# Kernel tuning notes

Measured on AMD Instinct MI355X. Metric: run time of the kernel, lower is better.

Reference implementation:

```python
import jax, jax.numpy as jnp
import numpy as np

B, T, D, H = 2, 2048, 2048, 16
HD = D // H  # 128
HALF = HD // 2  # 64


def _apply_rotary(x, cos, sin):
    """x: (B,H,T,HD); cos/sin: (T, HD//2). Interleaved rotation matching torch ref."""
    half = x.shape[-1] // 2
    x1, x2 = x[..., :half], x[..., half:]
    c = cos[None, None, :, :]
    s = sin[None, None, :, :]
    # stack on last axis then flatten -> out[...,2i]=x1*c-x2*s, out[...,2i+1]=x1*s+x2*c
    return jnp.stack([x1 * c - x2 * s, x1 * s + x2 * c], axis=-1).reshape(x.shape)


def setup_inputs() -> dict:
    key = jax.random.key(0)
    k1, k2, k3 = jax.random.split(key, 3)
    x = jax.random.normal(k1, (B, T, D), dtype=jnp.float32)
    # realistic RoPE tables: theta = 10000^{-2i/HD}
    inv_freq = 1.0 / (10000.0 ** (np.arange(0, HALF, dtype=np.float32) * 2.0 / HD))
    ang = np.arange(T, dtype=np.float32)[:, None] * inv_freq[None, :]  # (T, HALF)
    cos = jnp.asarray(np.cos(ang), dtype=jnp.float32)
    sin = jnp.asarray(np.sin(ang), dtype=jnp.float32)
    Wqkv = jax.random.normal(k2, (D, 3 * D), dtype=jnp.float32) * (D ** -0.5)
    Wproj = jax.random.normal(k3, (D, D), dtype=jnp.float32) * (D ** -0.5)
    return {"x": x, "cos": cos, "sin": sin, "Wqkv": Wqkv, "Wproj": Wproj}


def reference(x, cos, sin, Wqkv, Wproj):
    b, t, d = x.shape
    qkv = (x @ Wqkv).reshape(b, t, 3, H, HD)
    q = jnp.transpose(qkv[:, :, 0], (0, 2, 1, 3))  # (B,H,T,HD)
    k = jnp.transpose(qkv[:, :, 1], (0, 2, 1, 3))
    v = jnp.transpose(qkv[:, :, 2], (0, 2, 1, 3))
    q = _apply_rotary(q, cos, sin)
    k = _apply_rotary(k, cos, sin)
    scale = 1.0 / jnp.sqrt(jnp.asarray(HD, dtype=x.dtype))
    scores = jnp.einsum("bhqd,bhkd->bhqk", q, k) * scale
    causal = jnp.tril(jnp.ones((t, t), dtype=bool))
    scores = jnp.where(causal[None, None], scores, jnp.finfo(x.dtype).min)
    attn = jax.nn.softmax(scores, axis=-1)
    out = jnp.einsum("bhqk,bhkd->bhqd", attn, v)
    out = jnp.transpose(out, (0, 2, 1, 3)).reshape(b, t, d)
    return out @ Wproj
```

## Files before the change

### kernel.cpp

```cpp
#include <hip/hip_runtime.h>
#include <hip/hip_bf16.h>

#define B_  2
#define T_  2048
#define D_  2048
#define H_  16
#define HD_ 128
#define NT_ 4096
#define D3_ 6144

typedef __bf16 bf16;
typedef _Float16 f16;
typedef bf16 bf16x2 __attribute__((ext_vector_type(2)));
typedef bf16 bf16x4 __attribute__((ext_vector_type(4)));
typedef bf16 bf16x8 __attribute__((ext_vector_type(8)));
typedef f16  f16x2  __attribute__((ext_vector_type(2)));
typedef f16  f16x4  __attribute__((ext_vector_type(4)));
typedef float floatx4 __attribute__((ext_vector_type(4)));

__device__ __forceinline__ void gl_lds16(const void* g, void* l) {
    __builtin_amdgcn_global_load_lds((const __attribute__((address_space(1))) void*)g,
                                     (__attribute__((address_space(3))) void*)l, 16, 0, 0);
}

__global__ __launch_bounds__(256) void k_prep(const float* __restrict__ x,
                                              const float* __restrict__ Wqkv, const float* __restrict__ Wproj,
                                              bf16* __restrict__ xb, bf16* __restrict__ WqkvT, bf16* __restrict__ WprojT) {
    int blk = blockIdx.x;
    int tid = threadIdx.x;
    if (blk < 8192) {
        int i = blk * 256 + tid;
        float4 v = ((const float4*)x)[i];
        bf16x4 o = { (bf16)v.x, (bf16)v.y, (bf16)v.z, (bf16)v.w };
        ((bf16x4*)xb)[i] = o;
        return;
    }
    __shared__ float tile[64][65];
    const float* in; bf16* out; int C, bx;
    if (blk < 8192 + 3072) { bx = blk - 8192; in = Wqkv; out = WqkvT; C = D3_; }
    else                   { bx = blk - 8192 - 3072; in = Wproj; out = WprojT; C = D_; }
    const int R = D_;
    int nbx = C / 64;
    int c0 = (bx % nbx) * 64, r0 = (bx / nbx) * 64;
#pragma unroll
    for (int i = 0; i < 16; i++) {
        int idx = tid + i * 256, r = idx >> 6, c = idx & 63;
        tile[r][c] = in[(size_t)(r0 + r) * C + (c0 + c)];
    }
    __syncthreads();
#pragma unroll
    for (int i = 0; i < 16; i++) {
        int idx = tid + i * 256, r = idx >> 6, c = idx & 63;
        out[(size_t)(c0 + r) * R + (r0 + c)] = (bf16)tile[c][r];
    }
}

__global__ __launch_bounds__(512, 1) void k_gemm_qkv(const bf16* __restrict__ A, const bf16* __restrict__ Bt,
                                                     const float* __restrict__ cosp, const float* __restrict__ sinp,
                                                     bf16* __restrict__ Qg, bf16* __restrict__ Kg, f16* __restrict__ VTg) {
    __shared__ bf16 smem[3 * 24576];
    const int tid = threadIdx.x, wid = tid >> 6, lane = tid & 63;
    const int quad = lane >> 4, l16 = lane & 15;
    const int n0 = blockIdx.x * 128, m0 = blockIdx.y * 256;
    const int wr = (wid >> 1) * 64, wc = (wid & 1) * 64;
    const bf16* Ablk = A + (size_t)m0 * D_;
    const bf16* Bblk = Bt + (size_t)n0 * D_;
    const int sgch = (lane & 7) ^ (lane >> 3);
    const int aHalf = (wid >> 2) * 8192;
    const int rAbase = ((wid >> 1) & 1) * 64;
    const int coA = (rAbase + l16) * 64;
    const int coB = 16384 + (wc + l16) * 64;
    floatx4 acc[4][4] = {};

#define QKV_STAGE(KT, BUFO, JJ) do {                                                    \
        int cI_ = (JJ) * 512 + wid * 64 + lane;                                         \
        const bf16* gsrc_;                                                              \
        if ((JJ) < 4) gsrc_ = Ablk + (size_t)(cI_ >> 3) * D_ + (KT) * 64 + sgch * 8;    \
        else          gsrc_ = Bblk + (size_t)((cI_ >> 3) - 256) * D_ + (KT) * 64 + sgch * 8; \
        gl_lds16(gsrc_, smem + (BUFO) + ((JJ) * 512 + wid * 64) * 8);                   \
    } while (0)

#pragma unroll
    for (int j = 0; j < 6; j++) QKV_STAGE(0, 0, j);
#pragma unroll
    for (int j = 0; j < 6; j++) QKV_STAGE(1, 24576, j);
    asm volatile("s_waitcnt vmcnt(6)" ::: "memory");
    __builtin_amdgcn_s_barrier();

    int bcur = 0, bpre = 2;
    for (int t = 0; t < 32; t++) {
        const int bb = bcur * 24576;
        const int po = bpre * 24576;
        const int kpre = t + 2;
        const bool dopre = (kpre < 32);
        bf16x8 af[4][2], bfr0[2][2];
#pragma unroll
        for (int mt = 0; mt < 4; mt++)
#pragma unroll
            for (int kc = 0; kc < 2; kc++)
                af[mt][kc] = *(const bf16x8*)(smem + bb + aHalf + coA + mt * 1024 + (((kc * 4 + quad) ^ (l16 & 7)) * 8));
#pragma unroll
        for (int nt = 0; nt < 2; nt++)
#pragma unroll
            for (int kc = 0; kc < 2; kc++)
                bfr0[nt][kc] = *(const bf16x8*)(smem + bb + coB + nt * 1024 + (((kc * 4 + quad) ^ (l16 & 7)) * 8));
        if (dopre) { QKV_STAGE(kpre, po, 0); QKV_STAGE(kpre, po, 1); QKV_STAGE(kpre, po, 4); }
        __builtin_amdgcn_s_barrier();
        __builtin_amdgcn_s_setprio(1);
#pragma unroll
        for (int mt = 0; mt < 4; mt++)
#pragma unroll
            for (int nt = 0; nt < 2; nt++)
#pragma unroll
                for (int kc = 0; kc < 2; kc++)
                    acc[mt][nt] = __builtin_amdgcn_mfma_f32_16x16x32_bf16(af[mt][kc], bfr0[nt][kc], acc[mt][nt], 0, 0, 0);
        __builtin_amdgcn_s_setprio(0);
        __builtin_amdgcn_s_barrier();
        bf16x8 bfr1[2][2];
#pragma unroll
        for (int nt = 0; nt < 2; nt++)
#pragma unroll
            for (int kc = 0; kc < 2; kc++)
                bfr1[nt][kc] = *(const bf16x8*)(smem + bb + coB + (nt + 2) * 1024 + (((kc * 4 + quad) ^ (l16 & 7)) * 8));
        if (dopre) { QKV_STAGE(kpre, po, 2); QKV_STAGE(kpre, po, 3); QKV_STAGE(kpre, po, 5); }
        __builtin_amdgcn_s_barrier();
        __builtin_amdgcn_s_setprio(1);
#pragma unroll
        for (int mt = 0; mt < 4; mt++)
#pragma unroll
            for (int nt = 0; nt < 2; nt++)
#pragma unroll
                for (int kc = 0; kc < 2; kc++)
                    acc[mt][nt + 2] = __builtin_amdgcn_mfma_f32_16x16x32_bf16(af[mt][kc], bfr1[nt][kc], acc[mt][nt + 2], 0, 0, 0);
        __builtin_amdgcn_s_setprio(0);
        if (t == 30) asm volatile("s_waitcnt vmcnt(0)" ::: "memory");
        else         asm volatile("s_waitcnt vmcnt(6)" ::: "memory");
        __builtin_amdgcn_s_barrier();
        bcur = (bcur == 2) ? 0 : bcur + 1;
        bpre = (bpre == 2) ? 0 : bpre + 1;
    }
#undef QKV_STAGE

    bf16* const stage = smem;
#pragma unroll
    for (int mt = 0; mt < 4; mt++)
#pragma unroll
        for (int nt = 0; nt < 4; nt++)
#pragma unroll
            for (int r = 0; r < 4; r++)
                stage[(wr + mt * 16 + quad * 4 + r) * 130 + wc + nt * 16 + l16] = (bf16)acc[mt][nt][r];
    __syncthreads();
    const int type = n0 >> 11, h = (n0 & 2047) >> 7;
    const int b = m0 >> 11, t0 = m0 & 2047;
    if (type < 2) {
        bf16* out = (type == 0 ? Qg : Kg) + ((size_t)(b * H_ + h) * T_ + t0) * HD_;
#pragma unroll
        for (int it = 0; it < 32; it++) {
            int idx = it * 512 + tid, tl = idx >> 6, i = idx & 63;
            float c = cosp[(t0 + tl) * 64 + i], s = sinp[(t0 + tl) * 64 + i];
            float x1 = (float)stage[tl * 130 + i], x2 = (float)stage[tl * 130 + 64 + i];
            bf16x2 o = { (bf16)(x1 * c - x2 * s), (bf16)(x1 * s + x2 * c) };
            *(bf16x2*)(out + (size_t)tl * HD_ + 2 * i) = o;
        }
    } else {
        f16* out = VTg + (size_t)(b * H_ + h) * HD_ * T_ + t0;
#pragma unroll
        for (int it = 0; it < 32; it++) {
            int idx = it * 512 + tid, d = idx >> 7, tp = (idx & 127) * 2;
            f16x2 o = { (f16)(float)stage[tp * 130 + d], (f16)(float)stage[(tp + 1) * 130 + d] };
            *(f16x2*)(out + (size_t)d * T_ + tp) = o;
        }
    }
}

template <typename OutT>
__global__ __launch_bounds__(256) void k_gemm_bt(const bf16* __restrict__ A, const bf16* __restrict__ Bt,
                                                 OutT* __restrict__ C, int M, int N, int K) {
    __shared__ bf16 As[128 * 64];
    __shared__ bf16 Bs[128 * 64];
    const int tid = threadIdx.x, w = tid >> 6, lane = tid & 63;
    const int quad = lane >> 4, l16 = lane & 15;
    const int x7 = l16 & 7;
    const int n0 = blockIdx.x * 128, m0 = blockIdx.y * 128;
    const int wr = (w >> 1) * 64, wc = (w & 1) * 64;
    const bf16* Ab = A + (size_t)m0 * K;
    const bf16* Bb = Bt + (size_t)n0 * K;
    const int srow = lane >> 3, schunk = (lane & 7) ^ (lane >> 3);
    floatx4 acc[4][4] = {};
    for (int k0 = 0; k0 < K; k0 += 64) {
        __syncthreads();
#pragma unroll
        for (int i = 0; i < 4; i++) {
            int ch = w * 4 + i;
            int row = ch * 8 + srow;
            gl_lds16(Ab + (size_t)row * K + k0 + schunk * 8, As + ch * 512);
            gl_lds16(Bb + (size_t)row * K + k0 + schunk * 8, Bs + ch * 512);
        }
        __syncthreads();
#pragma unroll
        for (int kc = 0; kc < 2; kc++) {
            const int co = ((kc * 4 + quad) ^ x7) * 8;
            const bf16* Abase = As + (wr + l16) * 64 + co;
            const bf16* Bbase = Bs + (wc + l16) * 64 + co;
            bf16x8 af[4], bfr[4];
#pragma unroll
            for (int mt = 0; mt < 4; mt++) af[mt] = *(const bf16x8*)(Abase + mt * 1024);
#pragma unroll
            for (int nt = 0; nt < 4; nt++) bfr[nt] = *(const bf16x8*)(Bbase + nt * 1024);
#pragma unroll
            for (int mt = 0; mt < 4; mt++)
#pragma unroll
                for (int nt = 0; nt < 4; nt++)
                    acc[mt][nt] = __builtin_amdgcn_mfma_f32_16x16x32_bf16(af[mt], bfr[nt], acc[mt][nt], 0, 0, 0);
        }
    }
#pragma unroll
    for (int mt = 0; mt < 4; mt++)
#pragma unroll
        for (int nt = 0; nt < 4; nt++)
#pragma unroll
            for (int r = 0; r < 4; r++) {
                int row = m0 + wr + mt * 16 + quad * 4 + r;
                int col = n0 + wc + nt * 16 + l16;
                C[(size_t)row * N + col] = (OutT)acc[mt][nt][r];
            }
}

__global__ __launch_bounds__(256, 2) void k_flash(const bf16* __restrict__ Qg, const bf16* __restrict__ Kg,
                                                  const f16* __restrict__ VTg, bf16* __restrict__ Og) {
    __shared__ bf16 Ksh[2][64 * 128];
    __shared__ f16  Vsh[2][128 * 64];
    const int b1 = blockIdx.x;
    const int bh = b1 & 31;
    const int qt = (b1 < 256) ? (15 - (b1 >> 5)) : ((b1 - 256) >> 5);
    const int tid = threadIdx.x, w = tid >> 6, lane = tid & 63;
    const int quad = lane >> 4, l16 = lane & 15;
    const float scale2 = 0.08838834764831845f * 1.4426950408889634f;
    const int wrow = w * 32;
    const bf16* Kb = Kg + (size_t)bh * T_ * HD_;
    const f16*  Vb = VTg + (size_t)bh * HD_ * T_;
    const bf16* Qb = Qg + ((size_t)bh * T_ + qt * 128) * HD_;
    bf16x8 qf[2][4];
#pragma unroll
    for (int mt = 0; mt < 2; mt++)
#pragma unroll
        for (int kc = 0; kc < 4; kc++)
            qf[mt][kc] = *(const bf16x8*)(Qb + (size_t)(wrow + mt * 16 + l16) * HD_ + kc * 32 + quad * 8);
    floatx4 oaccT[8][2] = {};
    float lsum[2] = { 0.f, 0.f };
    const int nkt = 2 * (qt + 1);

    {
        const bf16* Kt = Kb;
        const f16*  Vt = Vb;
#pragma unroll
        for (int i = 0; i < 4; i++) {
            int ch = w * 4 + i;
            {
                int row = ch * 4 + (lane >> 4);
                int c = (lane & 15) ^ (row & 7);
                gl_lds16(Kt + (size_t)row * HD_ + c * 8, &Ksh[0][ch * 512]);
            }
            {
                int row = ch * 8 + (lane >> 3);
                int c = (lane & 7) ^ (row & 7);
                gl_lds16(Vt + (size_t)row * T_ + c * 8, &Vsh[0][ch * 512]);
            }
        }
    }
    int cur = 0;
    for (int kt = 0; kt < nkt; kt++) {
        __syncthreads();
        if (kt + 1 < nkt) {
            const bf16* Kt = Kb + (size_t)(kt + 1) * 64 * HD_;
            const f16*  Vt = Vb + (size_t)(kt + 1) * 64;
            const int nb = cur ^ 1;
#pragma unroll
            for (int i = 0; i < 4; i++) {
                int ch = w * 4 + i;
                {
                    int row = ch * 4 + (lane >> 4);
                    int c = (lane & 15) ^ (row & 7);
                    gl_lds16(Kt + (size_t)row * HD_ + c * 8, &Ksh[nb][ch * 512]);
                }
                {
                    int row = ch * 8 + (lane >> 3);
                    int c = (lane & 7) ^ (row & 7);
                    gl_lds16(Vt + (size_t)row * T_ + c * 8, &Vsh[nb][ch * 512]);
                }
            }
        }
        const bf16* Kcur = Ksh[cur];
        const f16*  Vcur = Vsh[cur];
        const bool diag = (kt >= 2 * qt);
        f16x4 pf[2][4];
#pragma unroll
        for (int nt = 0; nt < 4; nt++) {
            floatx4 s0 = {}, s1 = {};
#pragma unroll
            for (int kc = 0; kc < 4; kc++) {
                bf16x8 kf = *(const bf16x8*)(Kcur + (nt * 16 + l16) * 128 + (((kc * 4 + quad) ^ (l16 & 7)) * 8));
                s0 = __builtin_amdgcn_mfma_f32_16x16x32_bf16(kf, qf[0][kc], s0, 0, 0, 0);
                s1 = __builtin_amdgcn_mfma_f32_16x16x32_bf16(kf, qf[1][kc], s1, 0, 0, 0);
            }
#pragma unroll
            for (int r = 0; r < 4; r++) {
                float v0 = s0[r] * scale2, v1 = s1[r] * scale2;
                if (diag) {
                    int gk = kt * 64 + nt * 16 + quad * 4 + r;
                    if (gk > qt * 128 + wrow + l16) v0 = -1e30f;
                    if (gk > qt * 128 + wrow + 16 + l16) v1 = -1e30f;
                }
                float p0 = exp2f(v0), p1 = exp2f(v1);
                lsum[0] += p0; lsum[1] += p1;
                pf[0][nt][r] = (f16)p0; pf[1][nt][r] = (f16)p1;
            }
        }
#pragma unroll
        for (int nt = 0; nt < 4; nt++)
#pragma unroll
            for (int dt = 0; dt < 8; dt++) {
                int row = dt * 16 + l16;
                f16x4 vf = *(const f16x4*)(Vcur + row * 64 + (((nt * 2 + (quad >> 1)) ^ (row & 7)) * 8) + (quad & 1) * 4);
#pragma unroll
                for (int mt = 0; mt < 2; mt++)
                    oaccT[dt][mt] = __builtin_amdgcn_mfma_f32_16x16x16f16(vf, pf[mt][nt], oaccT[dt][mt], 0, 0, 0);
            }
        cur ^= 1;
    }
    const int b = bh >> 4, h = bh & 15;
    float inv[2];
#pragma unroll
    for (int mt = 0; mt < 2; mt++) {
        float l = lsum[mt];
        l += __shfl_xor(l, 16);
        l += __shfl_xor(l, 32);
        inv[mt] = 1.0f / l;
    }
#pragma unroll
    for (int mt = 0; mt < 2; mt++) {
        int t = qt * 128 + wrow + mt * 16 + l16;
#pragma unroll
        for (int dt = 0; dt < 8; dt++) {
            bf16x4 o;
#pragma unroll
            for (int r = 0; r < 4; r++) o[r] = (bf16)(oaccT[dt][mt][r] * inv[mt]);
            int c = h * HD_ + dt * 16 + quad * 4;
            *(bf16x4*)(Og + (size_t)(b * T_ + t) * D_ + c) = o;
        }
    }
}

extern "C" void kernel_launch(void* const* d_in, const int* in_sizes, int n_in,
                              void* d_out, int out_size, void* d_ws, size_t ws_size,
                              hipStream_t stream) {
    const float* x     = (const float*)d_in[0];
    const float* cosp  = (const float*)d_in[1];
    const float* sinp  = (const float*)d_in[2];
    const float* Wqkv  = (const float*)d_in[3];
    const float* Wproj = (const float*)d_in[4];
    float* out = (float*)d_out;
    char* ws = (char*)d_ws;
    bf16* xb     = (bf16*)(ws);
    bf16* WqkvT  = (bf16*)(ws + (size_t)(16u << 20));
    bf16* WprojT = (bf16*)(ws + (size_t)(40u << 20));
    bf16* Qg     = (bf16*)(ws + (size_t)(48u << 20));
    bf16* Kg     = (bf16*)(ws + (size_t)(64u << 20));
    f16*  VTg    = (f16*) (ws + (size_t)(80u << 20));
    bf16* Og     = xb;

    k_prep<<<dim3(8192 + 3072 + 1024), 256, 0, stream>>>(x, Wqkv, Wproj, xb, WqkvT, WprojT);
    k_gemm_qkv<<<dim3(D3_ / 128, NT_ / 256), 512, 0, stream>>>(xb, WqkvT, cosp, sinp, Qg, Kg, VTg);
    k_flash<<<dim3(512), 256, 0, stream>>>(Qg, Kg, VTg, Og);
    k_gemm_bt<float><<<dim3(D_ / 128, NT_ / 128), 256, 0, stream>>>(Og, WprojT, out, NT_, D_, D_);
}
```

Before: 377.6 us.

## Rewrite output projection GEMM with triple-buffered LDS pipeline and larger tiles

```diff
diff --git a/kernel.cpp b/kernel.cpp
--- a/kernel.cpp
+++ b/kernel.cpp
@@ -173,47 +173,91 @@
     }
 }
 
-template <typename OutT>
-__global__ __launch_bounds__(256) void k_gemm_bt(const bf16* __restrict__ A, const bf16* __restrict__ Bt,
-                                                 OutT* __restrict__ C, int M, int N, int K) {
-    __shared__ bf16 As[128 * 64];
-    __shared__ bf16 Bs[128 * 64];
-    const int tid = threadIdx.x, w = tid >> 6, lane = tid & 63;
+__global__ __launch_bounds__(512, 1) void k_proj(const bf16* __restrict__ A, const bf16* __restrict__ Bt,
+                                                 float* __restrict__ C) {
+    __shared__ bf16 smem[3 * 24576];
+    const int tid = threadIdx.x, wid = tid >> 6, lane = tid & 63;
     const int quad = lane >> 4, l16 = lane & 15;
-    const int x7 = l16 & 7;
-    const int n0 = blockIdx.x * 128, m0 = blockIdx.y * 128;
-    const int wr = (w >> 1) * 64, wc = (w & 1) * 64;
-    const bf16* Ab = A + (size_t)m0 * K;
-    const bf16* Bb = Bt + (size_t)n0 * K;
-    const int srow = lane >> 3, schunk = (lane & 7) ^ (lane >> 3);
+    const int n0 = blockIdx.x * 128, m0 = blockIdx.y * 256;
+    const int wr = (wid >> 1) * 64, wc = (wid & 1) * 64;
+    const bf16* Ablk = A + (size_t)m0 * D_;
+    const bf16* Bblk = Bt + (size_t)n0 * D_;
+    const int sgch = (lane & 7) ^ (lane >> 3);
+    const int aHalf = (wid >> 2) * 8192;
+    const int rAbase = ((wid >> 1) & 1) * 64;
+    const int coA = (rAbase + l16) * 64;
+    const int coB = 16384 + (wc + l16) * 64;
     floatx4 acc[4][4] = {};
-    for (int k0 = 0; k0 < K; k0 += 64) {
-        __syncthreads();
-#pragma unroll
-        for (int i = 0; i < 4; i++) {
-            int ch = w * 4 + i;
-            int row = ch * 8 + srow;
-            gl_lds16(Ab + (size_t)row * K + k0 + schunk * 8, As + ch * 512);
-            gl_lds16(Bb + (size_t)row * K + k0 + schunk * 8, Bs + ch * 512);
-        }
-        __syncthreads();
-#pragma unroll
-        for (int kc = 0; kc < 2; kc++) {
-            const int co = ((kc * 4 + quad) ^ x7) * 8;
-            const bf16* Abase = As + (wr + l16) * 64 + co;
-            const bf16* Bbase = Bs + (wc + l16) * 64 + co;
-            bf16x8 af[4], bfr[4];
-#pragma unroll
-            for (int mt = 0; mt < 4; mt++) af[mt] = *(const bf16x8*)(Abase + mt * 1024);
-#pragma unroll
-            for (int nt = 0; nt < 4; nt++) bfr[nt] = *(const bf16x8*)(Bbase + nt * 1024);
-#pragma unroll
-            for (int mt = 0; mt < 4; mt++)
-#pragma unroll
-                for (int nt = 0; nt < 4; nt++)
-                    acc[mt][nt] = __builtin_amdgcn_mfma_f32_16x16x32_bf16(af[mt], bfr[nt], acc[mt][nt], 0, 0, 0);
-        }
-    }
+
+#define PRJ_STAGE(KT, BUFO, JJ) do {                                                    \
+        int cI_ = (JJ) * 512 + wid * 64 + lane;                                         \
+        const bf16* gsrc_;                                                              \
+        if ((JJ) < 4) gsrc_ = Ablk + (size_t)(cI_ >> 3) * D_ + (KT) * 64 + sgch * 8;    \
+        else          gsrc_ = Bblk + (size_t)((cI_ >> 3) - 256) * D_ + (KT) * 64 + sgch * 8; \
+        gl_lds16(gsrc_, smem + (BUFO) + ((JJ) * 512 + wid * 64) * 8);                   \
+    } while (0)
+
+#pragma unroll
+    for (int j = 0; j < 6; j++) PRJ_STAGE(0, 0, j);
+#pragma unroll
+    for (int j = 0; j < 6; j++) PRJ_STAGE(1, 24576, j);
+    asm volatile("s_waitcnt vmcnt(6)" ::: "memory");
+    __builtin_amdgcn_s_barrier();
+
+    int bcur = 0, bpre = 2;
+    for (int t = 0; t < 32; t++) {
+        const int bb = bcur * 24576;
+        const int po = bpre * 24576;
+        const int kpre = t + 2;
+        const bool dopre = (kpre < 32);
+        bf16x8 af[4][2], bfr0[2][2];
+#pragma unroll
+        for (int mt = 0; mt < 4; mt++)
+#pragma unroll
+            for (int kc = 0; kc < 2; kc++)
+                af[mt][kc] = *(const bf16x8*)(smem + bb + aHalf + coA + mt * 1024 + (((kc * 4 + quad) ^ (l16 & 7)) * 8));
+#pragma unroll
+        for (int nt = 0; nt < 2; nt++)
+#pragma unroll
+            for (int kc = 0; kc < 2; kc++)
+                bfr0[nt][kc] = *(const bf16x8*)(smem + bb + coB + nt * 1024 + (((kc * 4 + quad) ^ (l16 & 7)) * 8));
+        if (dopre) { PRJ_STAGE(kpre, po, 0); PRJ_STAGE(kpre, po, 1); PRJ_STAGE(kpre, po, 4); }
+        __builtin_amdgcn_s_barrier();
+        __builtin_amdgcn_s_setprio(1);
+#pragma unroll
+        for (int mt = 0; mt < 4; mt++)
+#pragma unroll
+            for (int nt = 0; nt < 2; nt++)
+#pragma unroll
+                for (int kc = 0; kc < 2; kc++)
+                    acc[mt][nt] = __builtin_amdgcn_mfma_f32_16x16x32_bf16(af[mt][kc], bfr0[nt][kc], acc[mt][nt], 0, 0, 0);
+        __builtin_amdgcn_s_setprio(0);
+        __builtin_amdgcn_s_barrier();
+        bf16x8 bfr1[2][2];
+#pragma unroll
+        for (int nt = 0; nt < 2; nt++)
+#pragma unroll
+            for (int kc = 0; kc < 2; kc++)
+                bfr1[nt][kc] = *(const bf16x8*)(smem + bb + coB + (nt + 2) * 1024 + (((kc * 4 + quad) ^ (l16 & 7)) * 8));
+        if (dopre) { PRJ_STAGE(kpre, po, 2); PRJ_STAGE(kpre, po, 3); PRJ_STAGE(kpre, po, 5); }
+        __builtin_amdgcn_s_barrier();
+        __builtin_amdgcn_s_setprio(1);
+#pragma unroll
+        for (int mt = 0; mt < 4; mt++)
+#pragma unroll
+            for (int nt = 0; nt < 2; nt++)
+#pragma unroll
+                for (int kc = 0; kc < 2; kc++)
+                    acc[mt][nt + 2] = __builtin_amdgcn_mfma_f32_16x16x32_bf16(af[mt][kc], bfr1[nt][kc], acc[mt][nt + 2], 0, 0, 0);
+        __builtin_amdgcn_s_setprio(0);
+        if (t == 30) asm volatile("s_waitcnt vmcnt(0)" ::: "memory");
+        else         asm volatile("s_waitcnt vmcnt(6)" ::: "memory");
+        __builtin_amdgcn_s_barrier();
+        bcur = (bcur == 2) ? 0 : bcur + 1;
+        bpre = (bpre == 2) ? 0 : bpre + 1;
+    }
+#undef PRJ_STAGE
+
 #pragma unroll
     for (int mt = 0; mt < 4; mt++)
 #pragma unroll
@@ -222,7 +266,7 @@
             for (int r = 0; r < 4; r++) {
                 int row = m0 + wr + mt * 16 + quad * 4 + r;
                 int col = n0 + wc + nt * 16 + l16;
-                C[(size_t)row * N + col] = (OutT)acc[mt][nt][r];
+                C[(size_t)row * D_ + col] = acc[mt][nt][r];
             }
 }
 
@@ -372,5 +416,5 @@
     k_prep<<<dim3(8192 + 3072 + 1024), 256, 0, stream>>>(x, Wqkv, Wproj, xb, WqkvT, WprojT);
     k_gemm_qkv<<<dim3(D3_ / 128, NT_ / 256), 512, 0, stream>>>(xb, WqkvT, cosp, sinp, Qg, Kg, VTg);
     k_flash<<<dim3(512), 256, 0, stream>>>(Qg, Kg, VTg, Og);
-    k_gemm_bt<float><<<dim3(D_ / 128, NT_ / 128), 256, 0, stream>>>(Og, WprojT, out, NT_, D_, D_);
-}
+    k_proj<<<dim3(D_ / 128, NT_ / 256), 512, 0, stream>>>(Og, WprojT, out);
+}
```

Result: faster. 368.2 us (-2.5%).
